# Optimization experiments

Measured on AMD Instinct MI355X. Metric: run time of the kernel, lower is better.

Reference implementation:

```python
import jax, jax.numpy as jnp
import numpy as np

WS = 7       # window_size
SHIFT = 3    # shift
NH = 4       # n_heads


def _rel_index(ws: int) -> np.ndarray:
    # matches torch.cartesian_prod(arange(ws), arange(ws)) ordering (second index fastest)
    coords = np.stack(np.meshgrid(np.arange(ws), np.arange(ws), indexing='ij'), -1).reshape(-1, 2)
    d = coords[:, None, :] - coords[None, :, :]
    idx = (d[..., 0] + ws - 1) * (2 * ws - 1) + d[..., 1] + ws - 1
    return idx.reshape(-1).astype(np.int32)  # [ws*ws*ws*ws]


def _ln(x, g, b, eps=1e-5):
    m = x.mean(-1, keepdims=True)
    v = ((x - m) ** 2).mean(-1, keepdims=True)
    return (x - m) / jnp.sqrt(v + eps) * g + b


def setup_inputs() -> dict:
    key = jax.random.key(0)
    ks = jax.random.split(key, 14)
    B, H, W, C = 64, 56, 56, 128
    hidden = int(C * 4.0)
    s = 0.02
    return {
        'x': jax.random.normal(ks[0], (B, H, W, C), jnp.float32),
        'norm1_g': jnp.ones((C,), jnp.float32),
        'norm1_b': jnp.zeros((C,), jnp.float32),
        'qkv_w': jax.random.normal(ks[1], (3 * C, C), jnp.float32) * s,
        'qkv_b': jnp.zeros((3 * C,), jnp.float32),
        'out_w': jax.random.normal(ks[2], (C, C), jnp.float32) * s,
        'out_b': jnp.zeros((C,), jnp.float32),
        'pe_table': jax.random.normal(ks[3], (NH, (2 * WS - 1) ** 2), jnp.float32) * s,
        'norm2_g': jnp.ones((C,), jnp.float32),
        'norm2_b': jnp.zeros((C,), jnp.float32),
        'mlp_w1': jax.random.normal(ks[4], (hidden, C), jnp.float32) * s,
        'mlp_b1': jnp.zeros((hidden,), jnp.float32),
        'mlp_w2': jax.random.normal(ks[5], (C, hidden), jnp.float32) * s,
        'mlp_b2': jnp.zeros((C,), jnp.float32),
    }


def reference(x, norm1_g, norm1_b, qkv_w, qkv_b, out_w, out_b, pe_table,
              norm2_g, norm2_b, mlp_w1, mlp_b1, mlp_w2, mlp_b2):
    B, H, W, C = x.shape
    nH, nW = H // WS, W // WS
    L = WS * WS
    hd = C // NH

    h = _ln(x, norm1_g, norm1_b)
    h = jnp.roll(h, (SHIFT, SHIFT), (1, 2))  # shifted windows (no inverse roll in source)

    # window partition: [B,H,W,C] -> [B*nH*nW, L, C]
    h = h.reshape(B, nH, WS, nW, WS, C).transpose(0, 1, 3, 2, 4, 5).reshape(B * nH * nW, L, C)

    qkv = h @ qkv_w.T + qkv_b  # [N, L, 3C]
    q, k, v = jnp.split(qkv, 3, axis=-1)
    to_heads = lambda t: t.reshape(-1, L, NH, hd).transpose(0, 2, 1, 3)  # [N,h,L,hd]
    q, k, v = to_heads(q), to_heads(k), to_heads(v)

    idx = jnp.asarray(_rel_index(WS))
    bias = pe_table[:, idx].reshape(NH, L, L)  # gathered relative position bias

    scores = jnp.einsum('nhqd,nhkd->nhqk', q, k) / jnp.sqrt(jnp.float32(hd)) + bias[None]
    attn = jax.nn.softmax(scores, axis=-1)
    o = jnp.einsum('nhqk,nhkd->nhqd', attn, v).transpose(0, 2, 1, 3).reshape(-1, L, C)
    o = o @ out_w.T + out_b

    # window unpartition: [B*nH*nW, L, C] -> [B,H,W,C]
    o = o.reshape(B, nH, nW, WS, WS, C).transpose(0, 1, 3, 2, 4, 5).reshape(B, H, W, C)

    h2 = _ln(o, norm2_g, norm2_b)
    y = jax.nn.gelu(h2 @ mlp_w1.T + mlp_b1, approximate=False) @ mlp_w2.T + mlp_b2
    return y
```

## Files before the change

kernel.cpp:

```cpp
#include <hip/hip_runtime.h>
#include <hip/hip_bf16.h>


#define NWIN 4096
#define STR 40

typedef __attribute__((ext_vector_type(8))) short s8v;
typedef __attribute__((ext_vector_type(4))) float f4v;

__device__ __forceinline__ void split2(float v, unsigned short& h, unsigned short& l) {
    unsigned int b = __float_as_uint(v);
    h = (unsigned short)(b >> 16);
    float hf = __uint_as_float(b & 0xFFFF0000u);
    __hip_bfloat16 lo = __float2bfloat16(v - hf);
    l = *reinterpret_cast<unsigned short*>(&lo);
}
__device__ __forceinline__ unsigned short bfr(float v) {
    __hip_bfloat16 h = __float2bfloat16(v);
    return *reinterpret_cast<unsigned short*>(&h);
}
__device__ __forceinline__ float b2f(unsigned short u) {
    return __uint_as_float((unsigned int)u << 16);
}

__global__ __launch_bounds__(256) void presplit_kernel(
    const float* __restrict__ qkvw, const float* __restrict__ outw,
    const float* __restrict__ w1, const float* __restrict__ w2,
    unsigned short* __restrict__ P)
{
    int i = blockIdx.x * 256 + threadIdx.x;
    float v; unsigned short* ph; unsigned short* pl;
    if (i < 49152) {
        v = qkvw[i];
        if (i < 16384) v *= 0.17677669529663687f;
        ph = P + i; pl = P + 49152 + i;
    } else if (i < 65536) {
        int j = i - 49152; v = outw[j];
        ph = P + 98304 + j; pl = P + 114688 + j;
    } else if (i < 131072) {
        int j = i - 65536; v = w1[j];
        ph = P + 131072 + j; pl = P + 196608 + j;
    } else if (i < 196608) {
        int j = i - 131072; v = w2[j];
        ph = P + 262144 + j; pl = P + 327680 + j;
    } else return;
    unsigned short h, l; split2(v, h, l);
    *ph = h; *pl = l;
}

__global__ __launch_bounds__(256) void ln_kernel(
    const float* __restrict__ inF, const unsigned short* __restrict__ inH,
    const float* __restrict__ g, const float* __restrict__ bta,
    unsigned short* __restrict__ outH, unsigned short* __restrict__ outL,
    int mode, int tbase)
{
    int tid = threadIdx.x;
    int wave = tid >> 6, lane = tid & 63;
    int local = blockIdx.x * 4 + wave;
    float v0, v1;
    if (mode == 0) {
        int t = tbase + local;
        int n = t / 49, l = t - n * 49;
        int b = n >> 6, wh = (n >> 3) & 7, ww = n & 7;
        int i = l / 7, j = l - i * 7;
        int hh = wh * 7 + i, wimg = ww * 7 + j;
        int sh = (hh + 53) % 56, sw = (wimg + 53) % 56;
        const float* ip = inF + (size_t)((b * 56 + sh) * 56 + sw) * 128;
        v0 = ip[lane]; v1 = ip[lane + 64];
    } else {
        size_t o = (size_t)local * 128;
        v0 = b2f(inH[o + lane]);
        v1 = b2f(inH[o + lane + 64]);
    }
    float s = v0 + v1, sq = v0 * v0 + v1 * v1;
    #pragma unroll
    for (int off = 32; off > 0; off >>= 1) { s += __shfl_xor(s, off); sq += __shfl_xor(sq, off); }
    float mean = s * (1.0f / 128.0f);
    float var  = sq * (1.0f / 128.0f) - mean * mean;
    float rstd = rsqrtf(var + 1e-5f);
    float r0 = (v0 - mean) * rstd * g[lane]      + bta[lane];
    float r1 = (v1 - mean) * rstd * g[lane + 64] + bta[lane + 64];
    size_t o = (size_t)local * 128;
    if (mode == 0) {
        unsigned short h0, l0, h1, l1;
        split2(r0, h0, l0); split2(r1, h1, l1);
        outH[o + lane] = h0; outH[o + lane + 64] = h1;
        outL[o + lane] = l0; outL[o + lane + 64] = l1;
    } else {
        outH[o + lane] = bfr(r0); outH[o + lane + 64] = bfr(r1);
    }
}

template<int ASPLIT>
__global__ __launch_bounds__(256) void gemm_t(
    const unsigned short* __restrict__ Agh, const unsigned short* __restrict__ Agl,
    const unsigned short* __restrict__ Wgh, const unsigned short* __restrict__ Wgl,
    const float* __restrict__ bias,
    float* __restrict__ OutF, unsigned short* __restrict__ OutH,
    int M, int N, int K, int mode, int tbase)
{
    __shared__ __align__(16) unsigned short Ah[64 * STR];
    __shared__ __align__(16) unsigned short Al[(ASPLIT ? 64 : 1) * STR];
    __shared__ __align__(16) unsigned short Wh[64 * STR];
    __shared__ __align__(16) unsigned short Wl[64 * STR];
    int tid = threadIdx.x;
    int wv = tid >> 6, ln = tid & 63;
    int wm = wv & 1, wn = wv >> 1;
    int fm = ln & 15, fq = ln >> 4;
    int m0 = blockIdx.y * 64, n0 = blockIdx.x * 64;
    int sr = tid >> 2, sk = (tid & 3) * 8;
    int arow = m0 + sr; if (arow >= M) arow = M - 1;
    const unsigned short* pAh = Agh + (size_t)arow * K + sk;
    const unsigned short* pAl = ASPLIT ? (Agl + (size_t)arow * K + sk) : nullptr;
    const unsigned short* pWh = Wgh + (size_t)(n0 + sr) * K + sk;
    const unsigned short* pWl = Wgl + (size_t)(n0 + sr) * K + sk;
    int so = sr * STR + sk;

    f4v acc[2][2] = {};
    s8v ra, rl, rwh, rwl;
    #define LOADK(k0) do { \
        ra  = *reinterpret_cast<const s8v*>(pAh + (k0)); \
        if (ASPLIT) rl = *reinterpret_cast<const s8v*>(pAl + (k0)); \
        rwh = *reinterpret_cast<const s8v*>(pWh + (k0)); \
        rwl = *reinterpret_cast<const s8v*>(pWl + (k0)); } while (0)
    LOADK(0);
    for (int k0 = 0; k0 < K; k0 += 32) {
        *reinterpret_cast<s8v*>(&Ah[so]) = ra;
        if (ASPLIT) *reinterpret_cast<s8v*>(&Al[so]) = rl;
        *reinterpret_cast<s8v*>(&Wh[so]) = rwh;
        *reinterpret_cast<s8v*>(&Wl[so]) = rwl;
        __syncthreads();
        if (k0 + 32 < K) LOADK(k0 + 32);
        s8v fah[2], fal[2], fbh[2], fbl[2];
        #pragma unroll
        for (int t = 0; t < 2; ++t) {
            int ao = (wm * 32 + t * 16 + fm) * STR + fq * 8;
            fah[t] = *reinterpret_cast<const s8v*>(&Ah[ao]);
            if (ASPLIT) fal[t] = *reinterpret_cast<const s8v*>(&Al[ao]);
            int bo = (wn * 32 + t * 16 + fm) * STR + fq * 8;
            fbh[t] = *reinterpret_cast<const s8v*>(&Wh[bo]);
            fbl[t] = *reinterpret_cast<const s8v*>(&Wl[bo]);
        }
        #pragma unroll
        for (int tm = 0; tm < 2; ++tm)
            #pragma unroll
            for (int tn = 0; tn < 2; ++tn) {
                acc[tm][tn] = __builtin_amdgcn_mfma_f32_16x16x32_bf16(fah[tm], fbh[tn], acc[tm][tn], 0, 0, 0);
                acc[tm][tn] = __builtin_amdgcn_mfma_f32_16x16x32_bf16(fah[tm], fbl[tn], acc[tm][tn], 0, 0, 0);
                if (ASPLIT)
                    acc[tm][tn] = __builtin_amdgcn_mfma_f32_16x16x32_bf16(fal[tm], fbh[tn], acc[tm][tn], 0, 0, 0);
            }
        __syncthreads();
    }
    #undef LOADK

    #pragma unroll
    for (int tm = 0; tm < 2; ++tm)
        #pragma unroll
        for (int tn = 0; tn < 2; ++tn) {
            int col = n0 + wn * 32 + tn * 16 + fm;
            float bv = bias[col];
            if (mode == 2 && col < 128) bv *= 0.17677669529663687f;
            #pragma unroll
            for (int r = 0; r < 4; ++r) {
                int m = m0 + wm * 32 + tm * 16 + fq * 4 + r;
                if (m >= M) continue;
                float v = acc[tm][tn][r] + bv;
                if (mode == 1) v = 0.5f * v * (1.0f + erff(v * 0.70710678118654752f));
                if (mode == 3) {
                    int t = tbase + m;
                    int n = t / 49, l = t - n * 49;
                    int b = n >> 6, wh_ = (n >> 3) & 7, ww = n & 7;
                    int i = l / 7, j = l - i * 7;
                    size_t orow = (size_t)((b * 56 + wh_ * 7 + i) * 56 + ww * 7 + j);
                    OutF[orow * N + col] = v;
                } else {
                    OutH[(size_t)m * N + col] = bfr(v);
                }
            }
        }
}

__global__ void bias_tab_kernel(const float* __restrict__ pe, float* __restrict__ tab) {
    int t = threadIdx.x;
    int h = t >> 6, ln = t & 63;
    int g = ln >> 4, c = ln & 15;
    for (int mt = 0; mt < 4; ++mt)
        for (int nt = 0; nt < 4; ++nt)
            for (int r = 0; r < 4; ++r) {
                int l1 = mt * 16 + g * 4 + r, l2 = nt * 16 + c;
                float b = 0.f;
                if (l1 < 49 && l2 < 49) {
                    int i1 = l1 / 7, j1 = l1 % 7, i2 = l2 / 7, j2 = l2 % 7;
                    b = pe[h * 169 + (i1 - i2 + 6) * 13 + (j1 - j2 + 6)];
                }
                tab[((h * 64 + ln) * 16 + mt * 4 + nt) * 4 + r] = b;
            }
}

#define HB 7424
__global__ __launch_bounds__(256) void attn_mfma(
    const unsigned short* __restrict__ qkv,
    const float* __restrict__ btab,
    unsigned short* __restrict__ oH)
{
    __shared__ __align__(16) unsigned short lds[4 * HB];
    int tid = threadIdx.x;
    int win = blockIdx.x;
    const unsigned short* src = qkv + (size_t)win * 49 * 384;

    for (int i = tid; i < 1920; i += 256) {
        int hh = i / 480, rem = i % 480, d = rem / 15, l2 = 49 + rem % 15;
        lds[hh * HB + 5120 + d * 72 + l2] = 0;
    }
    for (int idx = tid; idx < 2352; idx += 256) {
        int l2 = idx / 48, c8 = idx - l2 * 48;
        int d8 = c8 * 8;
        s8v v8 = *reinterpret_cast<const s8v*>(src + (size_t)l2 * 384 + d8);
        int sec = d8 >> 7, dd = d8 & 127, hh = dd >> 5, kk = dd & 31;
        int base = hh * HB;
        if (sec <= 1) {
            *reinterpret_cast<s8v*>(&lds[base + sec * 2560 + l2 * 40 + kk]) = v8;
        } else {
            #pragma unroll
            for (int i = 0; i < 8; ++i)
                lds[base + 5120 + (kk + i) * 72 + l2] = (unsigned short)v8[i];
        }
    }
    __syncthreads();

    int h = tid >> 6, ln = tid & 63;
    int fm = ln & 15, fq = ln >> 4;
    int base = h * HB;

    s8v Qf[4], Kf[4];
    #pragma unroll
    for (int t = 0; t < 4; ++t) {
        Qf[t] = *reinterpret_cast<const s8v*>(&lds[base + (t * 16 + fm) * 40 + fq * 8]);
        Kf[t] = *reinterpret_cast<const s8v*>(&lds[base + 2560 + (t * 16 + fm) * 40 + fq * 8]);
    }
    f4v S[4][4] = {};
    #pragma unroll
    for (int mt = 0; mt < 4; ++mt)
        #pragma unroll
        for (int nt = 0; nt < 4; ++nt)
            S[mt][nt] = __builtin_amdgcn_mfma_f32_16x16x32_bf16(Qf[mt], Kf[nt], S[mt][nt], 0, 0, 0);
    #pragma unroll
    for (int mt = 0; mt < 4; ++mt)
        #pragma unroll
        for (int nt = 0; nt < 4; ++nt)
            S[mt][nt] += *reinterpret_cast<const f4v*>(&btab[((h * 64 + ln) * 16 + mt * 4 + nt) * 4]);

    float rcp[16];
    #pragma unroll
    for (int mt = 0; mt < 4; ++mt) {
        #pragma unroll
        for (int r = 0; r < 4; ++r) {
            float v0 = S[mt][0][r], v1 = S[mt][1][r], v2 = S[mt][2][r], v3 = S[mt][3][r];
            if (fm != 0) v3 = -1e30f;
            float mx = fmaxf(fmaxf(v0, v1), fmaxf(v2, v3));
            #pragma unroll
            for (int off = 1; off < 16; off <<= 1) mx = fmaxf(mx, __shfl_xor(mx, off));
            float e0 = __expf(v0 - mx), e1 = __expf(v1 - mx);
            float e2 = __expf(v2 - mx), e3 = __expf(v3 - mx);
            float sm = e0 + e1 + e2 + e3;
            #pragma unroll
            for (int off = 1; off < 16; off <<= 1) sm += __shfl_xor(sm, off);
            rcp[mt * 4 + r] = 1.0f / sm;
            int row = mt * 16 + fq * 4 + r;
            lds[base + row * 72 + 0 * 16 + fm]  = bfr(e0);
            lds[base + row * 72 + 1 * 16 + fm]  = bfr(e1);
            lds[base + row * 72 + 2 * 16 + fm]  = bfr(e2);
            lds[base + row * 72 + 3 * 16 + fm]  = bfr(e3);
        }
    }

    f4v O[4][2] = {};
    #pragma unroll
    for (int kt = 0; kt < 2; ++kt) {
        s8v Pf[4], Vf[2];
        #pragma unroll
        for (int mt = 0; mt < 4; ++mt)
            Pf[mt] = *reinterpret_cast<const s8v*>(&lds[base + (mt * 16 + fm) * 72 + kt * 32 + fq * 8]);
        #pragma unroll
        for (int nt = 0; nt < 2; ++nt)
            Vf[nt] = *reinterpret_cast<const s8v*>(&lds[base + 5120 + (nt * 16 + fm) * 72 + kt * 32 + fq * 8]);
        #pragma unroll
        for (int mt = 0; mt < 4; ++mt)
            #pragma unroll
            for (int nt = 0; nt < 2; ++nt)
                O[mt][nt] = __builtin_amdgcn_mfma_f32_16x16x32_bf16(Pf[mt], Vf[nt], O[mt][nt], 0, 0, 0);
    }

    size_t ob = (size_t)win * 49 * 128 + h * 32;
    #pragma unroll
    for (int mt = 0; mt < 4; ++mt)
        #pragma unroll
        for (int r = 0; r < 4; ++r) {
            int row = mt * 16 + fq * 4 + r;
            if (row < 49) {
                float sc = rcp[mt * 4 + r];
                #pragma unroll
                for (int nt = 0; nt < 2; ++nt)
                    oH[ob + (size_t)row * 128 + nt * 16 + fm] = bfr(O[mt][nt][r] * sc);
            }
        }
}

extern "C" void kernel_launch(void* const* d_in, const int* in_sizes, int n_in,
                              void* d_out, int out_size, void* d_ws, size_t ws_size,
                              hipStream_t stream) {
    const float* x    = (const float*)d_in[0];
    const float* n1g  = (const float*)d_in[1];
    const float* n1b  = (const float*)d_in[2];
    const float* qkvw = (const float*)d_in[3];
    const float* qkvb = (const float*)d_in[4];
    const float* outw = (const float*)d_in[5];
    const float* outb = (const float*)d_in[6];
    const float* pe   = (const float*)d_in[7];
    const float* n2g  = (const float*)d_in[8];
    const float* n2b  = (const float*)d_in[9];
    const float* w1   = (const float*)d_in[10];
    const float* b1   = (const float*)d_in[11];
    const float* w2   = (const float*)d_in[12];
    const float* b2   = (const float*)d_in[13];
    float* y = (float*)d_out;

    size_t wpc = NWIN;
    while (wpc > 8 && 851968 + wpc * 49 * 1536 > ws_size) wpc >>= 1;
    const int nchunks = (int)(NWIN / wpc);
    const size_t rows = wpc * 49;

    char* ws = (char*)d_ws;
    float* btab = (float*)ws;
    unsigned short* wpl = (unsigned short*)(ws + 65536);
    unsigned short* bufAh = (unsigned short*)(ws + 851968);
    unsigned short* bufAl = bufAh + rows * 128;
    unsigned short* bufBh = bufAl + rows * 128;
    const int gy = (int)((rows + 63) / 64);

    presplit_kernel<<<768, 256, 0, stream>>>(qkvw, outw, w1, w2, wpl);
    bias_tab_kernel<<<1, 256, 0, stream>>>(pe, btab);

    for (int c = 0; c < nchunks; ++c) {
        int tbase = (int)(c * wpc * 49);
        ln_kernel<<<(int)(rows / 4), 256, 0, stream>>>(
            x, nullptr, n1g, n1b, bufAh, bufAl, 0, tbase);
        gemm_t<1><<<dim3(6, gy), 256, 0, stream>>>(
            bufAh, bufAl, wpl, wpl + 49152, qkvb,
            nullptr, bufBh, (int)rows, 384, 128, 2, 0);
        attn_mfma<<<(int)wpc, 256, 0, stream>>>(bufBh, btab, bufAh);
        gemm_t<0><<<dim3(2, gy), 256, 0, stream>>>(
            bufAh, nullptr, wpl + 98304, wpl + 114688, outb,
            nullptr, bufBh, (int)rows, 128, 128, 0, 0);
        ln_kernel<<<(int)(rows / 4), 256, 0, stream>>>(
            nullptr, bufBh, n2g, n2b, bufAh, nullptr, 1, 0);
        gemm_t<0><<<dim3(8, gy), 256, 0, stream>>>(
            bufAh, nullptr, wpl + 131072, wpl + 196608, b1,
            nullptr, bufBh, (int)rows, 512, 128, 1, 0);
        gemm_t<0><<<dim3(2, gy), 256, 0, stream>>>(
            bufBh, nullptr, wpl + 262144, wpl + 327680, b2,
            y, nullptr, (int)rows, 128, 512, 3, tbase);
    }
}
```

Measured before the change: 739.3 us.

## Write V pre-transposed from QKV GEMM epilogue and vectorize attention LDS stores

The QKV GEMM epilogue now writes Q/K rows to a compact buffer and writes V directly into a per-window transposed, key-permuted layout. The attention kernel can then load V with 16-byte vector copies instead of scalar transposing stores into LDS. The key permutation lets each lane store its four softmax probabilities with one packed 8-byte write. The cost is scattered 2-byte global stores in the GEMM epilogue for the V columns, plus a larger workspace footprint and different buffer assignments.

```diff
diff --git a/kernel.cpp b/kernel.cpp
--- a/kernel.cpp
+++ b/kernel.cpp
@@ -4,6 +4,9 @@
 
 #define NWIN 4096
 #define STR 40
+#define HB 7440
+#define KOFF 2568
+#define VOFF 5136
 
 typedef __attribute__((ext_vector_type(8))) short s8v;
 typedef __attribute__((ext_vector_type(4))) float f4v;
@@ -97,6 +100,7 @@
     const unsigned short* __restrict__ Wgh, const unsigned short* __restrict__ Wgl,
     const float* __restrict__ bias,
     float* __restrict__ OutF, unsigned short* __restrict__ OutH,
+    unsigned short* __restrict__ OutV,
     int M, int N, int K, int mode, int tbase)
 {
     __shared__ __align__(16) unsigned short Ah[64 * STR];
@@ -160,7 +164,7 @@
         for (int tn = 0; tn < 2; ++tn) {
             int col = n0 + wn * 32 + tn * 16 + fm;
             float bv = bias[col];
-            if (mode == 2 && col < 128) bv *= 0.17677669529663687f;
+            if (mode == 4 && col < 128) bv *= 0.17677669529663687f;
             #pragma unroll
             for (int r = 0; r < 4; ++r) {
                 int m = m0 + wm * 32 + tm * 16 + fq * 4 + r;
@@ -174,6 +178,15 @@
                     int i = l / 7, j = l - i * 7;
                     size_t orow = (size_t)((b * 56 + wh_ * 7 + i) * 56 + ww * 7 + j);
                     OutF[orow * N + col] = v;
+                } else if (mode == 4) {
+                    if (col < 256) {
+                        OutH[(size_t)m * 256 + col] = bfr(v);
+                    } else {
+                        int dd = col - 256, hh = dd >> 5, d = dd & 31;
+                        int win = m / 49, l2 = m - win * 49;
+                        int kp = (l2 & 15) * 4 + (l2 >> 4);
+                        OutV[((size_t)win * 128 + hh * 32 + d) * 64 + kp] = bfr(v);
+                    }
                 } else {
                     OutH[(size_t)m * N + col] = bfr(v);
                 }
@@ -198,34 +211,35 @@
             }
 }
 
-#define HB 7424
 __global__ __launch_bounds__(256) void attn_mfma(
-    const unsigned short* __restrict__ qkv,
+    const unsigned short* __restrict__ qk,
+    const unsigned short* __restrict__ vt,
     const float* __restrict__ btab,
     unsigned short* __restrict__ oH)
 {
     __shared__ __align__(16) unsigned short lds[4 * HB];
     int tid = threadIdx.x;
     int win = blockIdx.x;
-    const unsigned short* src = qkv + (size_t)win * 49 * 384;
-
+    const unsigned short* srcqk = qk + (size_t)win * 49 * 256;
+    const unsigned short* srcv  = vt + (size_t)win * 8192;
+
+    for (int idx = tid; idx < 1568; idx += 256) {
+        int l2 = idx >> 5, c8 = idx & 31;
+        int d8 = c8 * 8;
+        s8v v8 = *reinterpret_cast<const s8v*>(srcqk + (size_t)l2 * 256 + d8);
+        int sec = d8 >> 7, dd = d8 & 127, hh = dd >> 5, kk = dd & 31;
+        *reinterpret_cast<s8v*>(&lds[hh * HB + (sec ? KOFF : 0) + l2 * 40 + kk]) = v8;
+    }
+    for (int idx = tid; idx < 1024; idx += 256) {
+        int row = idx >> 3, j = idx & 7;
+        s8v v8 = *reinterpret_cast<const s8v*>(srcv + (size_t)row * 64 + j * 8);
+        int hh = row >> 5, d = row & 31;
+        *reinterpret_cast<s8v*>(&lds[hh * HB + VOFF + d * 72 + j * 8]) = v8;
+    }
+    __syncthreads();
     for (int i = tid; i < 1920; i += 256) {
-        int hh = i / 480, rem = i % 480, d = rem / 15, l2 = 49 + rem % 15;
-        lds[hh * HB + 5120 + d * 72 + l2] = 0;
-    }
-    for (int idx = tid; idx < 2352; idx += 256) {
-        int l2 = idx / 48, c8 = idx - l2 * 48;
-        int d8 = c8 * 8;
-        s8v v8 = *reinterpret_cast<const s8v*>(src + (size_t)l2 * 384 + d8);
-        int sec = d8 >> 7, dd = d8 & 127, hh = dd >> 5, kk = dd & 31;
-        int base = hh * HB;
-        if (sec <= 1) {
-            *reinterpret_cast<s8v*>(&lds[base + sec * 2560 + l2 * 40 + kk]) = v8;
-        } else {
-            #pragma unroll
-            for (int i = 0; i < 8; ++i)
-                lds[base + 5120 + (kk + i) * 72 + l2] = (unsigned short)v8[i];
-        }
+        int hh = i / 480, rem = i % 480, d = rem / 15, j = rem % 15;
+        lds[hh * HB + VOFF + d * 72 + (j + 1) * 4 + 3] = 0;
     }
     __syncthreads();
 
@@ -237,7 +251,7 @@
     #pragma unroll
     for (int t = 0; t < 4; ++t) {
         Qf[t] = *reinterpret_cast<const s8v*>(&lds[base + (t * 16 + fm) * 40 + fq * 8]);
-        Kf[t] = *reinterpret_cast<const s8v*>(&lds[base + 2560 + (t * 16 + fm) * 40 + fq * 8]);
+        Kf[t] = *reinterpret_cast<const s8v*>(&lds[base + KOFF + (t * 16 + fm) * 40 + fq * 8]);
     }
     f4v S[4][4] = {};
     #pragma unroll
@@ -268,10 +282,8 @@
             for (int off = 1; off < 16; off <<= 1) sm += __shfl_xor(sm, off);
             rcp[mt * 4 + r] = 1.0f / sm;
             int row = mt * 16 + fq * 4 + r;
-            lds[base + row * 72 + 0 * 16 + fm]  = bfr(e0);
-            lds[base + row * 72 + 1 * 16 + fm]  = bfr(e1);
-            lds[base + row * 72 + 2 * 16 + fm]  = bfr(e2);
-            lds[base + row * 72 + 3 * 16 + fm]  = bfr(e3);
+            ushort4 pk = { bfr(e0), bfr(e1), bfr(e2), bfr(e3) };
+            *reinterpret_cast<ushort4*>(&lds[base + row * 72 + fm * 4]) = pk;
         }
     }
 
@@ -284,7 +296,7 @@
             Pf[mt] = *reinterpret_cast<const s8v*>(&lds[base + (mt * 16 + fm) * 72 + kt * 32 + fq * 8]);
         #pragma unroll
         for (int nt = 0; nt < 2; ++nt)
-            Vf[nt] = *reinterpret_cast<const s8v*>(&lds[base + 5120 + (nt * 16 + fm) * 72 + kt * 32 + fq * 8]);
+            Vf[nt] = *reinterpret_cast<const s8v*>(&lds[base + VOFF + (nt * 16 + fm) * 72 + kt * 32 + fq * 8]);
         #pragma unroll
         for (int mt = 0; mt < 4; ++mt)
             #pragma unroll
@@ -327,7 +339,7 @@
     float* y = (float*)d_out;
 
     size_t wpc = NWIN;
-    while (wpc > 8 && 851968 + wpc * 49 * 1536 > ws_size) wpc >>= 1;
+    while (wpc > 8 && 851968 + wpc * 116736ULL > ws_size) wpc >>= 1;
     const int nchunks = (int)(NWIN / wpc);
     const size_t rows = wpc * 49;
 
@@ -336,7 +348,9 @@
     unsigned short* wpl = (unsigned short*)(ws + 65536);
     unsigned short* bufAh = (unsigned short*)(ws + 851968);
     unsigned short* bufAl = bufAh + rows * 128;
-    unsigned short* bufBh = bufAl + rows * 128;
+    unsigned short* bufQK = bufAl + rows * 128;
+    unsigned short* bufV  = bufQK + rows * 256;
+    unsigned short* bufH  = bufV + wpc * 8192;
     const int gy = (int)((rows + 63) / 64);
 
     presplit_kernel<<<768, 256, 0, stream>>>(qkvw, outw, w1, w2, wpl);
@@ -348,18 +362,18 @@
             x, nullptr, n1g, n1b, bufAh, bufAl, 0, tbase);
         gemm_t<1><<<dim3(6, gy), 256, 0, stream>>>(
             bufAh, bufAl, wpl, wpl + 49152, qkvb,
-            nullptr, bufBh, (int)rows, 384, 128, 2, 0);
-        attn_mfma<<<(int)wpc, 256, 0, stream>>>(bufBh, btab, bufAh);
+            nullptr, bufQK, bufV, (int)rows, 384, 128, 4, 0);
+        attn_mfma<<<(int)wpc, 256, 0, stream>>>(bufQK, bufV, btab, bufAh);
         gemm_t<0><<<dim3(2, gy), 256, 0, stream>>>(
             bufAh, nullptr, wpl + 98304, wpl + 114688, outb,
-            nullptr, bufBh, (int)rows, 128, 128, 0, 0);
+            nullptr, bufAl, nullptr, (int)rows, 128, 128, 0, 0);
         ln_kernel<<<(int)(rows / 4), 256, 0, stream>>>(
-            nullptr, bufBh, n2g, n2b, bufAh, nullptr, 1, 0);
+            nullptr, bufAl, n2g, n2b, bufAh, nullptr, 1, 0);
         gemm_t<0><<<dim3(8, gy), 256, 0, stream>>>(
             bufAh, nullptr, wpl + 131072, wpl + 196608, b1,
-            nullptr, bufBh, (int)rows, 512, 128, 1, 0);
+            nullptr, bufH, nullptr, (int)rows, 512, 128, 1, 0);
         gemm_t<0><<<dim3(2, gy), 256, 0, stream>>>(
-            bufBh, nullptr, wpl + 262144, wpl + 327680, b2,
-            y, nullptr, (int)rows, 128, 512, 3, tbase);
-    }
-}
+            bufH, nullptr, wpl + 262144, wpl + 327680, b2,
+            y, nullptr, nullptr, (int)rows, 128, 512, 3, tbase);
+    }
+}
```

Result: slower. 786.9 us (+6.4%).
